# Optimization experiments

Hardware: AMD Instinct MI355X
Metric: run time of the kernel (lower is better)

## Reference

```python
import jax, jax.numpy as jnp
import numpy as np

INNER = 256   # inner_channel
NODES = 64    # nodes_num (prototypes)
EM_NUM = 3
DIAG_C = 128  # hardcoded diag_channel in FullyConnectGCLayer


def setup_inputs() -> dict:
    key = jax.random.key(0)
    ks = jax.random.split(key, 16)
    b, c, w, h = 4, 1024, 64, 64
    f32 = jnp.float32
    d = {}
    d["x"] = jax.random.normal(ks[0], (b, c, w, h), f32)
    # Conv2d weights re-initialized to N(0, 0.001) in Intra_graph.__init__
    d["W_in"] = 0.001 * jax.random.normal(ks[1], (INNER, c), f32)
    d["b_in"] = jnp.zeros((INNER,), f32)
    d["multi_proto"] = 0.001 * jax.random.normal(ks[2], (1, INNER, NODES), f32)
    d["pi0"] = jnp.ones((1, NODES), f32) / NODES
    # Conv1d layers keep default kaiming-uniform-ish init
    lim = 1.0 / np.sqrt(INNER)
    d["W_adj"] = jax.random.uniform(ks[3], (DIAG_C, INNER), f32, -lim, lim)
    d["b_adj"] = jax.random.uniform(ks[4], (DIAG_C,), f32, -lim, lim)
    d["W_diag"] = jax.random.uniform(ks[5], (DIAG_C, INNER), f32, -lim, lim)
    d["b_diag"] = jax.random.uniform(ks[6], (DIAG_C,), f32, -lim, lim)
    d["gcn_weight"] = 0.01 * jax.random.normal(ks[7], (INNER, INNER), f32)
    d["W_out"] = 0.001 * jax.random.normal(ks[8], (c, INNER), f32)
    d["b_out"] = jnp.zeros((c,), f32)
    d["gamma"] = jnp.ones((c,), f32)
    d["beta"] = jnp.zeros((c,), f32)
    d["W_out2"] = 0.001 * jax.random.normal(ks[9], (c, INNER), f32)
    d["b_out2"] = jnp.zeros((c,), f32)
    d["gamma2"] = jnp.ones((c,), f32)
    d["beta2"] = jnp.zeros((c,), f32)
    d["flag"] = 0
    return d


def _bn(y, g, bt):
    # BatchNorm2d in training mode: batch stats over (N,H,W), biased var, eps=1e-5
    m = jnp.mean(y, (0, 2, 3), keepdims=True)
    v = jnp.var(y, (0, 2, 3), keepdims=True)
    return (y - m) * jax.lax.rsqrt(v + 1e-5) * g[None, :, None, None] + bt[None, :, None, None]


def _forward(x, W_in, b_in, multi_proto, pi0, W_adj, b_adj, W_diag, b_diag,
             gcn_weight, W_out, b_out, gamma, beta, W_out2, b_out2, gamma2, beta2):
    b, c, w, h = x.shape
    wh = w * h
    x1 = (jnp.einsum('oi,bihw->bohw', W_in, x) + b_in[None, :, None, None]).reshape(b, INNER, wh)
    # ---- EM soft-clustering loop (runs under no_grad in torch) ----
    x1s = jax.lax.stop_gradient(x1)
    mu = jnp.broadcast_to(multi_proto, (b, INNER, NODES))
    pi = jnp.broadcast_to(pi0[None, :, :], (b, 1, NODES))
    for _ in range(EM_NUM):
        lik = jnp.einsum('bcm,bcn->bmn', x1s, mu)              # [b, wh, n]
        lik = jnp.exp(lik - jnp.max(lik, 2, keepdims=True))
        post = lik * pi
        post = post / (1e-18 + jnp.sum(post, 2, keepdims=True))
        prob = post / (1e-18 + jnp.sum(post, 1, keepdims=True))
        mu = jnp.einsum('bcm,bmn->bcn', x1s, prob)
        pi = jnp.sum(post, 1, keepdims=True) / wh
    post = jax.lax.stop_gradient(post)
    prob = jax.lax.stop_gradient(prob)
    # ---- aggregate to prototypes (grad flows through x1 only) ----
    x2 = jnp.einsum('bcm,bmn->bcn', x1, prob)                   # [b, inner, n]
    # ---- branch 2: scatter back, conv, bn ----
    x4 = jnp.einsum('bcn,bmn->bcm', x2, post).reshape(b, INNER, w, h)
    x4 = _bn(jnp.einsum('oi,bihw->bohw', W_out2, x4) + b_out2[None, :, None, None], gamma2, beta2)
    output2 = jax.nn.relu(jax.nn.relu(x4) + x)
    # ---- FullyConnectGCLayer on x2 ----
    xd = jnp.einsum('oi,bin->bon', W_diag, x2) + b_diag[None, :, None]
    dvec = jax.nn.sigmoid(jnp.mean(xd, 2))                      # [b, 128]
    xa = jnp.einsum('oi,bin->bon', W_adj, x2) + b_adj[None, :, None]  # [b, 128, n]
    # sigmoid(diag(d)) has 0.5 off-diagonal, sigmoid(d) on diagonal:
    # xa^T S xa = 0.5 * (1^T xa)^T (1^T xa) + xa^T diag(sig(d)-0.5) xa
    u = jnp.sum(xa, 1)                                          # [b, n]
    A = 0.5 * u[:, :, None] * u[:, None, :] + jnp.einsum('bcn,bc,bcm->bnm', xa, dvec - 0.5, xa)
    A = jax.nn.relu(A) + jnp.eye(NODES, dtype=x.dtype)[None]
    deg = jax.lax.stop_gradient(jnp.sum(A, 1) ** -0.5)          # no_grad degree, [b, n]
    A = deg[:, :, None] * A * deg[:, None, :]
    gout = jnp.einsum('oi,bin->bon', gcn_weight, jnp.einsum('bcn,bnm->bcm', x2, A))
    x2g = jax.nn.relu(gout) + x2                                # res_connect
    # ---- branch 1: scatter back, conv, bn ----
    x3 = jnp.einsum('bcn,bmn->bcm', x2g, post).reshape(b, INNER, w, h)
    x3 = _bn(jnp.einsum('oi,bihw->bohw', W_out, x3) + b_out[None, :, None, None], gamma, beta)
    output = jax.nn.relu(jax.nn.relu(x3) + x)
    return output, output2


def reference(x, W_in, b_in, multi_proto, pi0, W_adj, b_adj, W_diag, b_diag,
              gcn_weight, W_out, b_out, gamma, beta, W_out2, b_out2, gamma2, beta2, flag):
    # flag only gates a buffer EMA update (no effect on forward outputs)
    return _forward(x, W_in, b_in, multi_proto, pi0, W_adj, b_adj, W_diag, b_diag,
                    gcn_weight, W_out, b_out, gamma, beta, W_out2, b_out2, gamma2, beta2)
```

## Files before the change

kernel.cpp:

```cpp
#include <hip/hip_runtime.h>
#include <math.h>


typedef unsigned short u16;
typedef short s16x8 __attribute__((ext_vector_type(8)));
typedef float f32x4 __attribute__((ext_vector_type(4)));

constexpr int BB  = 4;
constexpr int CH  = 1024;
constexpr int IN  = 256;
constexpr int ND  = 64;
constexpr int WH  = 4096;
constexpr int DCN = 128;
constexpr size_t TOT = (size_t)BB * CH * WH;

__device__ inline u16 f2bf(float f) {
  unsigned u = __float_as_uint(f);
  return (u16)((u + 0x7fffu + ((u >> 16) & 1u)) >> 16);
}
__device__ inline s16x8 ld8(const u16* p) { return *(const s16x8*)p; }
#define MFMA16(a, b, c) __builtin_amdgcn_mfma_f32_16x16x32_bf16(a, b, c, 0, 0, 0)

__global__ void k_init(const float* __restrict__ Win, const float* __restrict__ mp,
                       const float* __restrict__ pi0, u16* __restrict__ Winb,
                       u16* __restrict__ mu_t, float* __restrict__ piw,
                       float* __restrict__ sp) {
  int idx = blockIdx.x * 256 + threadIdx.x;
  if (idx < IN * CH) { Winb[idx] = f2bf(Win[idx]); return; }
  int j = idx - IN * CH;
  if (j < BB * ND * IN) {
    int bb = j >> 14, n = (j >> 8) & 63, c = j & 255;
    mu_t[((size_t)(bb * ND + n)) * IN + c] = f2bf(mp[c * ND + n]);
    return;
  }
  j -= BB * ND * IN;
  if (j < BB * ND) { piw[j] = pi0[j & 63]; return; }
  j -= BB * ND;
  if (j < 3 * BB * ND) sp[j] = 0.f;
}

__global__ __launch_bounds__(512) void k_x1(
    const float* __restrict__ x, const u16* __restrict__ Winb,
    const float* __restrict__ bin, u16* __restrict__ x1, u16* __restrict__ x1t) {
  __shared__ u16 lt[64][40];
  const int t = threadIdx.x, w = t >> 6, lr = t & 15, lg = (t >> 4) & 3;
  const int wc = w & 3, wm = w >> 2;
  const int m0 = blockIdx.x * 64, b = blockIdx.y;
  const int si = t >> 4, sm = (t & 15) * 4;
  const float* xb = x + (size_t)b * CH * WH + m0 + sm;
  f32x4 acc[4][2];
#pragma unroll
  for (int i = 0; i < 4; ++i)
#pragma unroll
    for (int j = 0; j < 2; ++j) acc[i][j] = (f32x4){0.f, 0.f, 0.f, 0.f};
  const u16* wp = Winb + (size_t)(wc * 64 + lr) * CH + lg * 8;

  float4 nxt = *(const float4*)&xb[(size_t)si * WH];
  for (int k0 = 0; k0 < CH; k0 += 32) {
    float4 cur = nxt;
    __syncthreads();
    lt[sm + 0][si] = f2bf(cur.x); lt[sm + 1][si] = f2bf(cur.y);
    lt[sm + 2][si] = f2bf(cur.z); lt[sm + 3][si] = f2bf(cur.w);
    if (k0 + 32 < CH) nxt = *(const float4*)&xb[(size_t)(k0 + 32 + si) * WH];
    __syncthreads();
    s16x8 af[4], bf[2];
#pragma unroll
    for (int i = 0; i < 4; ++i) af[i] = ld8(wp + (size_t)i * 16 * CH + k0);
#pragma unroll
    for (int j = 0; j < 2; ++j) bf[j] = *(const s16x8*)&lt[wm * 32 + j * 16 + lr][lg * 8];
#pragma unroll
    for (int i = 0; i < 4; ++i)
#pragma unroll
      for (int j = 0; j < 2; ++j) acc[i][j] = MFMA16(af[i], bf[j], acc[i][j]);
  }
#pragma unroll
  for (int i = 0; i < 4; ++i) {
    const int cb = wc * 64 + i * 16 + lg * 4;
    const float4 bi = *(const float4*)&bin[cb];
    const float bia[4] = {bi.x, bi.y, bi.z, bi.w};
#pragma unroll
    for (int j = 0; j < 2; ++j) {
      const int m = m0 + wm * 32 + j * 16 + lr;
      float v[4];
#pragma unroll
      for (int r = 0; r < 4; ++r) v[r] = acc[i][j][r] + bia[r];
      ushort4 o;
      o.x = f2bf(v[0]); o.y = f2bf(v[1]); o.z = f2bf(v[2]); o.w = f2bf(v[3]);
      *(ushort4*)&x1t[((size_t)b * WH + m) * IN + cb] = o;
#pragma unroll
      for (int r = 0; r < 4; ++r)
        x1[((size_t)b * IN + cb + r) * WH + m] = f2bf(v[r]);
    }
  }
}

__global__ __launch_bounds__(256) void k_em(
    const u16* __restrict__ x1, const u16* __restrict__ x1t,
    const u16* __restrict__ mu_t, const float* __restrict__ piw,
    float* __restrict__ sp, u16* __restrict__ pmn,
    float* __restrict__ mup, float* __restrict__ gp, int doG) {
  __shared__ u16 ptl[64][72];
  const int t = threadIdx.x, w = t >> 6, lr = t & 15, lg = (t >> 4) & 3;
  const int mch = blockIdx.x, b = blockIdx.y;
  {
    f32x4 acc[4];
#pragma unroll
    for (int f = 0; f < 4; ++f) acc[f] = (f32x4){0.f, 0.f, 0.f, 0.f};
    const u16* ap = x1t + ((size_t)b * WH + mch * 64 + w * 16 + lr) * IN + lg * 8;
    const u16* bp = mu_t + ((size_t)b * ND + lr) * IN + lg * 8;
#pragma unroll
    for (int k0 = 0; k0 < IN; k0 += 32) {
      s16x8 a = ld8(ap + k0);
#pragma unroll
      for (int f = 0; f < 4; ++f)
        acc[f] = MFMA16(a, ld8(bp + f * 16 * IN + k0), acc[f]);
    }
    float pi_[4], spart[4] = {0.f, 0.f, 0.f, 0.f};
#pragma unroll
    for (int f = 0; f < 4; ++f) pi_[f] = piw[b * ND + f * 16 + lr];
#pragma unroll
    for (int r = 0; r < 4; ++r) {
      float v0 = acc[0][r], v1 = acc[1][r], v2 = acc[2][r], v3 = acc[3][r];
      float mx = fmaxf(fmaxf(v0, v1), fmaxf(v2, v3));
      mx = fmaxf(mx, __shfl_xor(mx, 1)); mx = fmaxf(mx, __shfl_xor(mx, 2));
      mx = fmaxf(mx, __shfl_xor(mx, 4)); mx = fmaxf(mx, __shfl_xor(mx, 8));
      float e0 = __expf(v0 - mx) * pi_[0], e1 = __expf(v1 - mx) * pi_[1];
      float e2 = __expf(v2 - mx) * pi_[2], e3 = __expf(v3 - mx) * pi_[3];
      float s = e0 + e1 + e2 + e3;
      s += __shfl_xor(s, 1); s += __shfl_xor(s, 2);
      s += __shfl_xor(s, 4); s += __shfl_xor(s, 8);
      const float inv = 1.f / (1e-18f + s);
      e0 *= inv; e1 *= inv; e2 *= inv; e3 *= inv;
      const int mloc = w * 16 + lg * 4 + r;
      const size_t gbase = ((size_t)b * WH + mch * 64 + mloc) * ND + lr;
      u16 q0 = f2bf(e0), q1 = f2bf(e1), q2 = f2bf(e2), q3 = f2bf(e3);
      pmn[gbase + 0]  = q0; pmn[gbase + 16] = q1;
      pmn[gbase + 32] = q2; pmn[gbase + 48] = q3;
      ptl[0 + lr][mloc]  = q0; ptl[16 + lr][mloc] = q1;
      ptl[32 + lr][mloc] = q2; ptl[48 + lr][mloc] = q3;
      spart[0] += e0; spart[1] += e1; spart[2] += e2; spart[3] += e3;
    }
#pragma unroll
    for (int f = 0; f < 4; ++f) {
      spart[f] += __shfl_xor(spart[f], 16);
      spart[f] += __shfl_xor(spart[f], 32);
    }
    if (((t >> 4) & 3) == 0) {
#pragma unroll
      for (int f = 0; f < 4; ++f)
        atomicAdd(&sp[b * ND + f * 16 + lr], spart[f]);
    }
  }
  __syncthreads();
  {
    f32x4 acc[4][4];
#pragma unroll
    for (int i = 0; i < 4; ++i)
#pragma unroll
      for (int j = 0; j < 4; ++j) acc[i][j] = (f32x4){0.f, 0.f, 0.f, 0.f};
    const u16* ap = x1 + ((size_t)b * IN + w * 64 + lr) * WH + mch * 64 + lg * 8;
#pragma unroll
    for (int ks = 0; ks < 2; ++ks) {
      s16x8 af[4], bf[4];
#pragma unroll
      for (int i = 0; i < 4; ++i) af[i] = ld8(ap + (size_t)i * 16 * WH + ks * 32);
#pragma unroll
      for (int j = 0; j < 4; ++j)
        bf[j] = *(const s16x8*)&ptl[j * 16 + lr][ks * 32 + lg * 8];
#pragma unroll
      for (int i = 0; i < 4; ++i)
#pragma unroll
        for (int j = 0; j < 4; ++j) acc[i][j] = MFMA16(af[i], bf[j], acc[i][j]);
    }
    float* mo = mup + ((size_t)mch * BB + b) * (IN * ND);
#pragma unroll
    for (int i = 0; i < 4; ++i)
#pragma unroll
      for (int j = 0; j < 4; ++j)
#pragma unroll
        for (int r = 0; r < 4; ++r) {
          const int c = w * 64 + i * 16 + lg * 4 + r, n = j * 16 + lr;
          mo[c * ND + n] = acc[i][j][r];
        }
  }
  if (doG) {
    f32x4 acc[4];
#pragma unroll
    for (int j = 0; j < 4; ++j) acc[j] = (f32x4){0.f, 0.f, 0.f, 0.f};
#pragma unroll
    for (int ks = 0; ks < 2; ++ks) {
      s16x8 a = *(const s16x8*)&ptl[w * 16 + lr][ks * 32 + lg * 8];
#pragma unroll
      for (int j = 0; j < 4; ++j) {
        s16x8 bq = *(const s16x8*)&ptl[j * 16 + lr][ks * 32 + lg * 8];
        acc[j] = MFMA16(a, bq, acc[j]);
      }
    }
    float* go = gp + ((size_t)mch * BB + b) * (ND * ND);
#pragma unroll
    for (int j = 0; j < 4; ++j)
#pragma unroll
      for (int r = 0; r < 4; ++r) {
        const int n1 = w * 16 + lg * 4 + r, n2 = j * 16 + lr;
        go[n1 * ND + n2] = acc[j][r];
      }
  }
}

__global__ void k_mu_red(const float* __restrict__ mup, const float* __restrict__ spb,
                         float* __restrict__ piw, float* __restrict__ mu,
                         u16* __restrict__ mu_t, const float* __restrict__ gp,
                         float* __restrict__ G, int doG) {
  const int idx = blockIdx.x * 256 + threadIdx.x;
  const int bb = idx >> 14, c = (idx >> 6) & 255, n = idx & 63;
  float s = 0.f;
#pragma unroll 8
  for (int ch = 0; ch < 64; ++ch)
    s += mup[((size_t)ch * BB + bb) * (IN * ND) + (idx & 16383)];
  const float v = s / (1e-18f + spb[bb * ND + n]);
  mu[idx] = v;
  mu_t[((size_t)(bb * ND + n)) * IN + c] = f2bf(v);
  if (idx < BB * ND) piw[idx] = spb[idx] * (1.f / (float)WH);
  if (doG && idx < BB * ND * ND) {
    float g = 0.f;
#pragma unroll 8
    for (int ch = 0; ch < 64; ++ch) g += gp[(size_t)ch * (BB * ND * ND) + idx];
    G[idx] = g;
  }
}

__global__ __launch_bounds__(256) void k_gcA(
    const float* __restrict__ mu, const float* __restrict__ gw,
    const float* __restrict__ Wa, const float* __restrict__ ba,
    const float* __restrict__ Wd, const float* __restrict__ bd,
    float* __restrict__ qbuf, float* __restrict__ xabuf, float* __restrict__ dv) {
  __shared__ float sx2[IN * ND];
  __shared__ float srm[IN];
  const int t = threadIdx.x, blk = blockIdx.x, b = blockIdx.y;
  if (blk < 6) {
    const float* src = mu + (size_t)b * IN * ND;
#pragma unroll
    for (int q4 = 0; q4 < 16; ++q4)
      *(float4*)&sx2[q4 * 1024 + t * 4] = *(const float4*)&src[q4 * 1024 + t * 4];
    __syncthreads();
    const int rg = t >> 4, cg = t & 15;
    const float* W = (blk < 4) ? gw + (size_t)(blk * 64 + rg * 4) * IN
                               : Wa + (size_t)((blk - 4) * 64 + rg * 4) * IN;
    float acc[4][4] = {};
    for (int i4 = 0; i4 < 64; ++i4) {
      float4 xv[4];
#pragma unroll
      for (int e = 0; e < 4; ++e)
        xv[e] = *(const float4*)&sx2[(i4 * 4 + e) * 64 + cg * 4];
#pragma unroll
      for (int rr = 0; rr < 4; ++rr) {
        const float4 w4 = *(const float4*)&W[(size_t)rr * IN + i4 * 4];
        acc[rr][0] += w4.x * xv[0].x + w4.y * xv[1].x + w4.z * xv[2].x + w4.w * xv[3].x;
        acc[rr][1] += w4.x * xv[0].y + w4.y * xv[1].y + w4.z * xv[2].y + w4.w * xv[3].y;
        acc[rr][2] += w4.x * xv[0].z + w4.y * xv[1].z + w4.z * xv[2].z + w4.w * xv[3].z;
        acc[rr][3] += w4.x * xv[0].w + w4.y * xv[1].w + w4.z * xv[2].w + w4.w * xv[3].w;
      }
    }
    if (blk < 4) {
      float* dst = qbuf + (size_t)b * IN * ND + (size_t)(blk * 64 + rg * 4) * ND + cg * 4;
#pragma unroll
      for (int rr = 0; rr < 4; ++rr)
        *(float4*)&dst[(size_t)rr * ND] =
            make_float4(acc[rr][0], acc[rr][1], acc[rr][2], acc[rr][3]);
    } else {
      const int xr = (blk - 4) * 64 + rg * 4;
      float* dst = xabuf + (size_t)b * DCN * ND + (size_t)xr * ND + cg * 4;
#pragma unroll
      for (int rr = 0; rr < 4; ++rr) {
        const float bv = ba[xr + rr];
        *(float4*)&dst[(size_t)rr * ND] =
            make_float4(acc[rr][0] + bv, acc[rr][1] + bv, acc[rr][2] + bv, acc[rr][3] + bv);
      }
    }
  } else {
    {
      const float* row = mu + (size_t)b * IN * ND + (size_t)t * ND;
      float s = 0.f;
#pragma unroll
      for (int n4 = 0; n4 < 16; ++n4) {
        float4 v = *(const float4*)&row[n4 * 4];
        s += v.x + v.y + v.z + v.w;
      }
      srm[t] = s * (1.f / ND);
    }
    __syncthreads();
    if (t < DCN) {
      float a = 0.f;
#pragma unroll
      for (int i4 = 0; i4 < 64; ++i4) {
        float4 w4 = *(const float4*)&Wd[(size_t)t * IN + i4 * 4];
        float4 r4 = *(const float4*)&srm[i4 * 4];
        a += w4.x * r4.x + w4.y * r4.y + w4.z * r4.z + w4.w * r4.w;
      }
      a += bd[t];
      dv[b * DCN + t] = 1.f / (1.f + __expf(-a)) - 0.5f;
    }
  }
}

__global__ __launch_bounds__(256) void k_gcB(
    const float* __restrict__ xabuf, const float* __restrict__ dv,
    float* __restrict__ ahat) {
  __shared__ float sxa[DCN * ND];
  __shared__ float sdv[DCN];
  __shared__ float su[ND];
  __shared__ float sdeg[ND];
  __shared__ float sA[ND * 65];
  const int t = threadIdx.x, b = blockIdx.x;
  const float* src = xabuf + (size_t)b * DCN * ND;
#pragma unroll
  for (int q4 = 0; q4 < 8; ++q4)
    *(float4*)&sxa[q4 * 1024 + t * 4] = *(const float4*)&src[q4 * 1024 + t * 4];
  if (t < DCN) sdv[t] = dv[b * DCN + t];
  __syncthreads();
  if (t < ND) {
    float s = 0.f;
    for (int dc = 0; dc < DCN; ++dc) s += sxa[dc * ND + t];
    su[t] = s;
  }
  __syncthreads();
  {
    const int n1g = t >> 4, n2g = t & 15;
    float acc[4][4] = {};
    for (int dc = 0; dc < DCN; ++dc) {
      const float dvv = sdv[dc];
      float4 v1 = *(const float4*)&sxa[dc * ND + n1g * 4];
      const float4 v2 = *(const float4*)&sxa[dc * ND + n2g * 4];
      v1.x *= dvv; v1.y *= dvv; v1.z *= dvv; v1.w *= dvv;
      acc[0][0] += v1.x * v2.x; acc[0][1] += v1.x * v2.y;
      acc[0][2] += v1.x * v2.z; acc[0][3] += v1.x * v2.w;
      acc[1][0] += v1.y * v2.x; acc[1][1] += v1.y * v2.y;
      acc[1][2] += v1.y * v2.z; acc[1][3] += v1.y * v2.w;
      acc[2][0] += v1.z * v2.x; acc[2][1] += v1.z * v2.y;
      acc[2][2] += v1.z * v2.z; acc[2][3] += v1.z * v2.w;
      acc[3][0] += v1.w * v2.x; acc[3][1] += v1.w * v2.y;
      acc[3][2] += v1.w * v2.z; acc[3][3] += v1.w * v2.w;
    }
#pragma unroll
    for (int i = 0; i < 4; ++i) {
      const int n1 = n1g * 4 + i;
      const float u1 = su[n1];
#pragma unroll
      for (int j = 0; j < 4; ++j) {
        const int n2 = n2g * 4 + j;
        const float v = acc[i][j] + 0.5f * u1 * su[n2];
        sA[n1 * 65 + n2] = fmaxf(v, 0.f) + (n1 == n2 ? 1.f : 0.f);
      }
    }
  }
  __syncthreads();
  if (t < ND) {
    float s = 0.f;
    for (int m = 0; m < ND; ++m) s += sA[m * 65 + t];
    sdeg[t] = rsqrtf(s);
  }
  __syncthreads();
  {
    const int n1g = t >> 4, n2g = t & 15;
#pragma unroll
    for (int i = 0; i < 4; ++i) {
      const int n1 = n1g * 4 + i;
      const float dr = sdeg[n1];
      float4 o;
      o.x = dr * sA[n1 * 65 + n2g * 4 + 0] * sdeg[n2g * 4 + 0];
      o.y = dr * sA[n1 * 65 + n2g * 4 + 1] * sdeg[n2g * 4 + 1];
      o.z = dr * sA[n1 * 65 + n2g * 4 + 2] * sdeg[n2g * 4 + 2];
      o.w = dr * sA[n1 * 65 + n2g * 4 + 3] * sdeg[n2g * 4 + 3];
      *(float4*)&ahat[(size_t)b * ND * ND + n1 * ND + n2g * 4] = o;
    }
  }
}

__global__ __launch_bounds__(256) void k_gcC(
    const float* __restrict__ qbuf, const float* __restrict__ ahat,
    const float* __restrict__ mu, float* __restrict__ x2g) {
  __shared__ float sq[64 * 68];
  __shared__ float sAh[64 * 65];
  const int t = threadIdx.x, ro = blockIdx.x * 64, b = blockIdx.y;
  {
    const int r = t >> 2, seg = (t & 3) * 16;
    const float* qs = qbuf + (size_t)b * IN * ND + (size_t)(ro + r) * ND + seg;
#pragma unroll
    for (int f = 0; f < 4; ++f) {
      float4 v = *(const float4*)&qs[f * 4];
      sq[r * 68 + seg + f * 4 + 0] = v.x; sq[r * 68 + seg + f * 4 + 1] = v.y;
      sq[r * 68 + seg + f * 4 + 2] = v.z; sq[r * 68 + seg + f * 4 + 3] = v.w;
    }
    const float* as = ahat + (size_t)b * ND * ND + (size_t)r * ND + seg;
#pragma unroll
    for (int f = 0; f < 4; ++f) {
      float4 v = *(const float4*)&as[f * 4];
      sAh[r * 65 + seg + f * 4 + 0] = v.x; sAh[r * 65 + seg + f * 4 + 1] = v.y;
      sAh[r * 65 + seg + f * 4 + 2] = v.z; sAh[r * 65 + seg + f * 4 + 3] = v.w;
    }
  }
  __syncthreads();
  const int rg = t >> 4, cg = t & 15;
  float acc[4][4] = {};
  for (int k = 0; k < ND; ++k) {
    const float4 a4 = *(const float4*)&sAh[k * 65 + cg * 4];
    float qv[4];
#pragma unroll
    for (int rr = 0; rr < 4; ++rr) qv[rr] = sq[(rg * 4 + rr) * 68 + k];
#pragma unroll
    for (int rr = 0; rr < 4; ++rr) {
      acc[rr][0] += qv[rr] * a4.x; acc[rr][1] += qv[rr] * a4.y;
      acc[rr][2] += qv[rr] * a4.z; acc[rr][3] += qv[rr] * a4.w;
    }
  }
#pragma unroll
  for (int rr = 0; rr < 4; ++rr) {
    const size_t off = (size_t)b * IN * ND + (size_t)(ro + rg * 4 + rr) * ND + cg * 4;
    const float4 xv = *(const float4*)&mu[off];
    float4 o;
    o.x = fmaxf(acc[rr][0], 0.f) + xv.x; o.y = fmaxf(acc[rr][1], 0.f) + xv.y;
    o.z = fmaxf(acc[rr][2], 0.f) + xv.z; o.w = fmaxf(acc[rr][3], 0.f) + xv.w;
    *(float4*)&x2g[off] = o;
  }
}

__global__ __launch_bounds__(256) void k_zdual(
    const float* __restrict__ Wo, const float* __restrict__ v1,
    float* __restrict__ z1o, u16* __restrict__ zb1o,
    const float* __restrict__ Wo2, const float* __restrict__ v2,
    float* __restrict__ z2o, u16* __restrict__ zb2o) {
  const float* W = blockIdx.z ? Wo2 : Wo;
  const float* v = blockIdx.z ? v2 : v1;
  float* z  = blockIdx.z ? z2o : z1o;
  u16* zb   = blockIdx.z ? zb2o : zb1o;
  __shared__ float As[16][68];
  __shared__ float Bs[16][64];
  const int t = threadIdx.x, tx = t & 15, ty = t >> 4;
  const int o0 = blockIdx.x * 64, bb = blockIdx.y;
  const int aoo = t >> 2, akq = (t & 3) * 4;
  const int bkk = t >> 4, bnq = (t & 15) * 4;
  float acc[4][4] = {};
  for (int k0 = 0; k0 < IN; k0 += 16) {
    {
      float4 w4 = *(const float4*)&W[(size_t)(o0 + aoo) * IN + k0 + akq];
      As[akq + 0][aoo] = w4.x; As[akq + 1][aoo] = w4.y;
      As[akq + 2][aoo] = w4.z; As[akq + 3][aoo] = w4.w;
    }
    *(float4*)&Bs[bkk][bnq] = *(const float4*)&v[((size_t)bb * IN + k0 + bkk) * ND + bnq];
    __syncthreads();
#pragma unroll
    for (int kk = 0; kk < 16; ++kk) {
      float4 a4 = *(const float4*)&As[kk][ty * 4];
      float4 b4 = *(const float4*)&Bs[kk][tx * 4];
      float ar[4] = {a4.x, a4.y, a4.z, a4.w}, br[4] = {b4.x, b4.y, b4.z, b4.w};
#pragma unroll
      for (int i = 0; i < 4; ++i)
#pragma unroll
        for (int j = 0; j < 4; ++j) acc[i][j] += ar[i] * br[j];
    }
    __syncthreads();
  }
#pragma unroll
  for (int i = 0; i < 4; ++i) {
    float4 r = make_float4(acc[i][0], acc[i][1], acc[i][2], acc[i][3]);
    const size_t off = ((size_t)bb * CH + o0 + ty * 4 + i) * ND + tx * 4;
    *(float4*)&z[off] = r;
    ushort4 h;
    h.x = f2bf(r.x); h.y = f2bf(r.y); h.z = f2bf(r.z); h.w = f2bf(r.w);
    *(ushort4*)&zb[off] = h;
  }
}

__global__ __launch_bounds__(256) void k_stats(
    const float* __restrict__ z1, const float* __restrict__ z2,
    const float* __restrict__ sp, const float* __restrict__ G,
    const float* __restrict__ gam, const float* __restrict__ bet,
    const float* __restrict__ gam2, const float* __restrict__ bet2,
    float* __restrict__ abc) {
  const int t = threadIdx.x;
  const int o = blockIdx.x * 4 + (t >> 6), lane = t & 63;
#pragma unroll
  for (int br = 0; br < 2; ++br) {
    const float* z = br ? z2 : z1;
    float macc = 0.f, eacc = 0.f;
    for (int bb = 0; bb < BB; ++bb) {
      const float zv = z[((size_t)bb * CH + o) * ND + lane];
      float s1 = zv * sp[bb * ND + lane];
      const float* Gb = G + (size_t)bb * ND * ND;
      float gz = 0.f;
      for (int k = 0; k < ND; ++k) {
        const float zk = __shfl(zv, k);
        gz += Gb[k * ND + lane] * zk;
      }
      float q = zv * gz;
#pragma unroll
      for (int off = 32; off; off >>= 1) {
        s1 += __shfl_xor(s1, off);
        q  += __shfl_xor(q, off);
      }
      macc += s1; eacc += q;
    }
    const float inv = 1.f / (float)((size_t)BB * WH);
    const float mean = macc * inv;
    const float var  = eacc * inv - mean * mean;
    const float a = (br ? gam2[o] : gam[o]) * rsqrtf(var + 1e-5f);
    const float c = (br ? bet2[o] : bet[o]) - mean * a;
    if (lane == 0) { abc[br * 2 * CH + o] = a; abc[br * 2 * CH + CH + o] = c; }
  }
}

__global__ __launch_bounds__(256) void k_epi(
    const u16* __restrict__ zb1, const u16* __restrict__ zb2,
    const u16* __restrict__ post, const float* __restrict__ abc,
    const float* __restrict__ x, float* __restrict__ out1, float* __restrict__ out2) {
  const int t = threadIdx.x, w = t >> 6, lr = t & 15, lg = (t >> 4) & 3;
  const int m0 = blockIdx.x * 256 + w * 64, o0 = blockIdx.y * 64, bb = blockIdx.z;
  f32x4 acc1[4][4], acc2[4][4];
#pragma unroll
  for (int i = 0; i < 4; ++i)
#pragma unroll
    for (int j = 0; j < 4; ++j) {
      acc1[i][j] = (f32x4){0.f, 0.f, 0.f, 0.f};
      acc2[i][j] = (f32x4){0.f, 0.f, 0.f, 0.f};
    }
  const u16* z1p = zb1 + ((size_t)bb * CH + o0 + lr) * ND + lg * 8;
  const u16* z2p = zb2 + ((size_t)bb * CH + o0 + lr) * ND + lg * 8;
  const u16* pp  = post + ((size_t)bb * WH + m0 + lr) * ND + lg * 8;
#pragma unroll
  for (int ks = 0; ks < 2; ++ks) {
    s16x8 a1[4], a2[4], bq[4];
#pragma unroll
    for (int i = 0; i < 4; ++i) {
      a1[i] = ld8(z1p + i * 16 * ND + ks * 32);
      a2[i] = ld8(z2p + i * 16 * ND + ks * 32);
    }
#pragma unroll
    for (int j = 0; j < 4; ++j) bq[j] = ld8(pp + j * 16 * ND + ks * 32);
#pragma unroll
    for (int i = 0; i < 4; ++i)
#pragma unroll
      for (int j = 0; j < 4; ++j) {
        acc1[i][j] = MFMA16(a1[i], bq[j], acc1[i][j]);
        acc2[i][j] = MFMA16(a2[i], bq[j], acc2[i][j]);
      }
  }
#pragma unroll
  for (int i = 0; i < 4; ++i)
#pragma unroll
    for (int r = 0; r < 4; ++r) {
      const int o = o0 + i * 16 + lg * 4 + r;
      const float a1v = abc[o], c1v = abc[CH + o];
      const float a2v = abc[2 * CH + o], c2v = abc[3 * CH + o];
      const size_t base = ((size_t)bb * CH + o) * WH + m0 + lr;
#pragma unroll
      for (int j = 0; j < 4; ++j) {
        const size_t off = base + j * 16;
        const float xv = x[off];
        out1[off] = fmaxf(fmaxf(a1v * acc1[i][j][r] + c1v, 0.f) + xv, 0.f);
        out2[off] = fmaxf(fmaxf(a2v * acc2[i][j][r] + c2v, 0.f) + xv, 0.f);
      }
    }
}

extern "C" void kernel_launch(void* const* d_in, const int* in_sizes, int n_in,
                              void* d_out, int out_size, void* d_ws, size_t ws_size,
                              hipStream_t stream) {
  (void)in_sizes; (void)n_in; (void)out_size; (void)ws_size;
  const float* x    = (const float*)d_in[0];
  const float* Win  = (const float*)d_in[1];
  const float* bin  = (const float*)d_in[2];
  const float* mp   = (const float*)d_in[3];
  const float* pi0  = (const float*)d_in[4];
  const float* Wa   = (const float*)d_in[5];
  const float* ba   = (const float*)d_in[6];
  const float* Wd   = (const float*)d_in[7];
  const float* bd   = (const float*)d_in[8];
  const float* gw   = (const float*)d_in[9];
  const float* Wo   = (const float*)d_in[10];
  const float* gam  = (const float*)d_in[12];
  const float* bet  = (const float*)d_in[13];
  const float* Wo2  = (const float*)d_in[14];
  const float* gam2 = (const float*)d_in[16];
  const float* bet2 = (const float*)d_in[17];

  char* ob = (char*)d_out;
  char* wp = (char*)d_ws;
  float* mup = (float*)(ob + 0);
  float* gp  = (float*)(ob + 16777216);
  float* z1  = (float*)(ob + 20971520);
  float* z2  = (float*)(ob + 22020096);
  u16*   x1    = (u16*)(wp + 0);
  u16*   x1t   = (u16*)(wp + 8388608);
  u16*   Winb  = (u16*)(wp + 16777216);
  u16*   mu_t  = (u16*)(wp + 17301504);
  u16*   pmn   = (u16*)(wp + 17432576);
  float* mu    = (float*)(wp + 19529728);
  float* x2g   = (float*)(wp + 19791872);
  u16*   zb1   = (u16*)(wp + 20054016);
  u16*   zb2   = (u16*)(wp + 20578304);
  float* sp3   = (float*)(wp + 21102592);
  float* piw   = (float*)(wp + 21105664);
  float* abc   = (float*)(wp + 21106688);
  float* G     = (float*)(wp + 21123072);
  float* qbuf  = (float*)(wp + 21188608);
  float* xabuf = (float*)(wp + 21450752);
  float* dvb   = (float*)(wp + 21581824);
  float* ahat  = (float*)(wp + 21583872);
  float* out1  = (float*)d_out;
  float* out2  = out1 + TOT;

  k_init<<<dim3(1284), 256, 0, stream>>>(Win, mp, pi0, Winb, mu_t, piw, sp3);
  k_x1<<<dim3(64, BB), 512, 0, stream>>>(x, Winb, bin, x1, x1t);
  for (int it = 0; it < 3; ++it) {
    float* spb = sp3 + it * 256;
    const int doG = (it == 2);
    k_em<<<dim3(64, BB), 256, 0, stream>>>(x1, x1t, mu_t, piw, spb, pmn, mup, gp, doG);
    k_mu_red<<<dim3(256), 256, 0, stream>>>(mup, spb, piw, mu, mu_t, gp, G, doG);
  }
  k_gcA<<<dim3(7, BB), 256, 0, stream>>>(mu, gw, Wa, ba, Wd, bd, qbuf, xabuf, dvb);
  k_gcB<<<dim3(BB), 256, 0, stream>>>(xabuf, dvb, ahat);
  k_gcC<<<dim3(4, BB), 256, 0, stream>>>(qbuf, ahat, mu, x2g);
  k_zdual<<<dim3(16, BB, 2), 256, 0, stream>>>(Wo, x2g, z1, zb1, Wo2, mu, z2, zb2);
  k_stats<<<dim3(256), 256, 0, stream>>>(z1, z2, sp3 + 512, G, gam, bet, gam2, bet2, abc);
  k_epi<<<dim3(16, 16, BB), 256, 0, stream>>>(zb1, zb2, pmn, abc, x, out1, out2);
}
```

Baseline: 232.9 us.

## Coalesce x1 stores via LDS, store EM partials in bf16, skip redundant pmn writes

k_x1 now stages the channel-major x1 tile in shared memory and writes it out as coalesced 16-byte rows, replacing scattered 2-byte stores. The EM kernel writes its per-chunk mu and G partial sums as bf16 instead of fp32, which halves the scratch traffic read back by k_mu_red. It also writes the responsibility matrix pmn only on the last iteration, since only that one is consumed. The cost is lower precision in the partial sums before reduction, plus extra LDS use in k_x1 that may reduce occupancy.

```diff
diff --git a/kernel.cpp b/kernel.cpp
--- a/kernel.cpp
+++ b/kernel.cpp
@@ -18,6 +18,7 @@
   unsigned u = __float_as_uint(f);
   return (u16)((u + 0x7fffu + ((u >> 16) & 1u)) >> 16);
 }
+__device__ inline float bf2f(u16 u) { return __uint_as_float((unsigned)u << 16); }
 __device__ inline s16x8 ld8(const u16* p) { return *(const s16x8*)p; }
 #define MFMA16(a, b, c) __builtin_amdgcn_mfma_f32_16x16x32_bf16(a, b, c, 0, 0, 0)
 
@@ -43,6 +44,7 @@
     const float* __restrict__ x, const u16* __restrict__ Winb,
     const float* __restrict__ bin, u16* __restrict__ x1, u16* __restrict__ x1t) {
   __shared__ u16 lt[64][40];
+  __shared__ u16 st[256][72];
   const int t = threadIdx.x, w = t >> 6, lr = t & 15, lg = (t >> 4) & 3;
   const int wc = w & 3, wm = w >> 2;
   const int m0 = blockIdx.x * 64, b = blockIdx.y;
@@ -80,17 +82,25 @@
     const float bia[4] = {bi.x, bi.y, bi.z, bi.w};
 #pragma unroll
     for (int j = 0; j < 2; ++j) {
-      const int m = m0 + wm * 32 + j * 16 + lr;
+      const int ml = wm * 32 + j * 16 + lr;
       float v[4];
 #pragma unroll
       for (int r = 0; r < 4; ++r) v[r] = acc[i][j][r] + bia[r];
       ushort4 o;
       o.x = f2bf(v[0]); o.y = f2bf(v[1]); o.z = f2bf(v[2]); o.w = f2bf(v[3]);
-      *(ushort4*)&x1t[((size_t)b * WH + m) * IN + cb] = o;
-#pragma unroll
-      for (int r = 0; r < 4; ++r)
-        x1[((size_t)b * IN + cb + r) * WH + m] = f2bf(v[r]);
-    }
+      *(ushort4*)&x1t[((size_t)b * WH + m0 + ml) * IN + cb] = o;
+      st[cb + 0][ml] = o.x; st[cb + 1][ml] = o.y;
+      st[cb + 2][ml] = o.z; st[cb + 3][ml] = o.w;
+    }
+  }
+  __syncthreads();
+  {
+    const int c = t >> 1, mh = (t & 1) * 32;
+    u16* dst = &x1[((size_t)b * IN + c) * WH + m0 + mh];
+    const u16* src = &st[c][mh];
+#pragma unroll
+    for (int q = 0; q < 4; ++q)
+      *(uint4*)(dst + q * 8) = *(const uint4*)(src + q * 8);
   }
 }
 
@@ -98,7 +108,7 @@
     const u16* __restrict__ x1, const u16* __restrict__ x1t,
     const u16* __restrict__ mu_t, const float* __restrict__ piw,
     float* __restrict__ sp, u16* __restrict__ pmn,
-    float* __restrict__ mup, float* __restrict__ gp, int doG) {
+    u16* __restrict__ mup16, u16* __restrict__ gp16, int doLast) {
   __shared__ u16 ptl[64][72];
   const int t = threadIdx.x, w = t >> 6, lr = t & 15, lg = (t >> 4) & 3;
   const int mch = blockIdx.x, b = blockIdx.y;
@@ -110,10 +120,10 @@
     const u16* bp = mu_t + ((size_t)b * ND + lr) * IN + lg * 8;
 #pragma unroll
     for (int k0 = 0; k0 < IN; k0 += 32) {
-      s16x8 a = ld8(ap + k0);
+      s16x8 av = ld8(ap + k0);
 #pragma unroll
       for (int f = 0; f < 4; ++f)
-        acc[f] = MFMA16(a, ld8(bp + f * 16 * IN + k0), acc[f]);
+        acc[f] = MFMA16(av, ld8(bp + f * 16 * IN + k0), acc[f]);
     }
     float pi_[4], spart[4] = {0.f, 0.f, 0.f, 0.f};
 #pragma unroll
@@ -132,12 +142,14 @@
       const float inv = 1.f / (1e-18f + s);
       e0 *= inv; e1 *= inv; e2 *= inv; e3 *= inv;
       const int mloc = w * 16 + lg * 4 + r;
-      const size_t gbase = ((size_t)b * WH + mch * 64 + mloc) * ND + lr;
       u16 q0 = f2bf(e0), q1 = f2bf(e1), q2 = f2bf(e2), q3 = f2bf(e3);
-      pmn[gbase + 0]  = q0; pmn[gbase + 16] = q1;
-      pmn[gbase + 32] = q2; pmn[gbase + 48] = q3;
       ptl[0 + lr][mloc]  = q0; ptl[16 + lr][mloc] = q1;
       ptl[32 + lr][mloc] = q2; ptl[48 + lr][mloc] = q3;
+      if (doLast) {
+        const size_t gbase = ((size_t)b * WH + mch * 64 + mloc) * ND + lr;
+        pmn[gbase + 0]  = q0; pmn[gbase + 16] = q1;
+        pmn[gbase + 32] = q2; pmn[gbase + 48] = q3;
+      }
       spart[0] += e0; spart[1] += e1; spart[2] += e2; spart[3] += e3;
     }
 #pragma unroll
@@ -172,7 +184,7 @@
 #pragma unroll
         for (int j = 0; j < 4; ++j) acc[i][j] = MFMA16(af[i], bf[j], acc[i][j]);
     }
-    float* mo = mup + ((size_t)mch * BB + b) * (IN * ND);
+    u16* mo = mup16 + ((size_t)mch * BB + b) * (IN * ND);
 #pragma unroll
     for (int i = 0; i < 4; ++i)
 #pragma unroll
@@ -180,43 +192,43 @@
 #pragma unroll
         for (int r = 0; r < 4; ++r) {
           const int c = w * 64 + i * 16 + lg * 4 + r, n = j * 16 + lr;
-          mo[c * ND + n] = acc[i][j][r];
+          mo[c * ND + n] = f2bf(acc[i][j][r]);
         }
   }
-  if (doG) {
+  if (doLast) {
     f32x4 acc[4];
 #pragma unroll
     for (int j = 0; j < 4; ++j) acc[j] = (f32x4){0.f, 0.f, 0.f, 0.f};
 #pragma unroll
     for (int ks = 0; ks < 2; ++ks) {
-      s16x8 a = *(const s16x8*)&ptl[w * 16 + lr][ks * 32 + lg * 8];
+      s16x8 av = *(const s16x8*)&ptl[w * 16 + lr][ks * 32 + lg * 8];
 #pragma unroll
       for (int j = 0; j < 4; ++j) {
         s16x8 bq = *(const s16x8*)&ptl[j * 16 + lr][ks * 32 + lg * 8];
-        acc[j] = MFMA16(a, bq, acc[j]);
-      }
-    }
-    float* go = gp + ((size_t)mch * BB + b) * (ND * ND);
+        acc[j] = MFMA16(av, bq, acc[j]);
+      }
+    }
+    u16* go = gp16 + ((size_t)mch * BB + b) * (ND * ND);
 #pragma unroll
     for (int j = 0; j < 4; ++j)
 #pragma unroll
       for (int r = 0; r < 4; ++r) {
         const int n1 = w * 16 + lg * 4 + r, n2 = j * 16 + lr;
-        go[n1 * ND + n2] = acc[j][r];
-      }
-  }
-}
-
-__global__ void k_mu_red(const float* __restrict__ mup, const float* __restrict__ spb,
+        go[n1 * ND + n2] = f2bf(acc[j][r]);
+      }
+  }
+}
+
+__global__ void k_mu_red(const u16* __restrict__ mup16, const float* __restrict__ spb,
                          float* __restrict__ piw, float* __restrict__ mu,
-                         u16* __restrict__ mu_t, const float* __restrict__ gp,
+                         u16* __restrict__ mu_t, const u16* __restrict__ gp16,
                          float* __restrict__ G, int doG) {
   const int idx = blockIdx.x * 256 + threadIdx.x;
   const int bb = idx >> 14, c = (idx >> 6) & 255, n = idx & 63;
   float s = 0.f;
 #pragma unroll 8
   for (int ch = 0; ch < 64; ++ch)
-    s += mup[((size_t)ch * BB + bb) * (IN * ND) + (idx & 16383)];
+    s += bf2f(mup16[((size_t)ch * BB + bb) * (IN * ND) + (idx & 16383)]);
   const float v = s / (1e-18f + spb[bb * ND + n]);
   mu[idx] = v;
   mu_t[((size_t)(bb * ND + n)) * IN + c] = f2bf(v);
@@ -224,7 +236,8 @@
   if (doG && idx < BB * ND * ND) {
     float g = 0.f;
 #pragma unroll 8
-    for (int ch = 0; ch < 64; ++ch) g += gp[(size_t)ch * (BB * ND * ND) + idx];
+    for (int ch = 0; ch < 64; ++ch)
+      g += bf2f(gp16[(size_t)ch * (BB * ND * ND) + idx]);
     G[idx] = g;
   }
 }
@@ -585,10 +598,10 @@
 
   char* ob = (char*)d_out;
   char* wp = (char*)d_ws;
-  float* mup = (float*)(ob + 0);
-  float* gp  = (float*)(ob + 16777216);
-  float* z1  = (float*)(ob + 20971520);
-  float* z2  = (float*)(ob + 22020096);
+  u16*   mup16 = (u16*)(ob + 0);
+  u16*   gp16  = (u16*)(ob + 8388608);
+  float* z1    = (float*)(ob + 10485760);
+  float* z2    = (float*)(ob + 11534336);
   u16*   x1    = (u16*)(wp + 0);
   u16*   x1t   = (u16*)(wp + 8388608);
   u16*   Winb  = (u16*)(wp + 16777216);
@@ -613,9 +626,11 @@
   k_x1<<<dim3(64, BB), 512, 0, stream>>>(x, Winb, bin, x1, x1t);
   for (int it = 0; it < 3; ++it) {
     float* spb = sp3 + it * 256;
-    const int doG = (it == 2);
-    k_em<<<dim3(64, BB), 256, 0, stream>>>(x1, x1t, mu_t, piw, spb, pmn, mup, gp, doG);
-    k_mu_red<<<dim3(256), 256, 0, stream>>>(mup, spb, piw, mu, mu_t, gp, G, doG);
+    const int doLast = (it == 2);
+    k_em<<<dim3(64, BB), 256, 0, stream>>>(x1, x1t, mu_t, piw, spb, pmn,
+                                           mup16, gp16, doLast);
+    k_mu_red<<<dim3(256), 256, 0, stream>>>(mup16, spb, piw, mu, mu_t,
+                                            gp16, G, doLast);
   }
   k_gcA<<<dim3(7, BB), 256, 0, stream>>>(mu, gw, Wa, ba, Wd, bd, qbuf, xabuf, dvb);
   k_gcB<<<dim3(BB), 256, 0, stream>>>(xabuf, dvb, ahat);
```

Result: faster. 227.0 us (-2.5%).
